# Kernel optimization log

Measured on AMD Instinct MI355X. Metric: run time of the kernel, lower is better.

## Reference

```python
import jax, jax.numpy as jnp
import numpy as np

VOCAB = 32000
D_MODEL = 1024


def setup_inputs() -> dict:
    key = jax.random.key(0)
    k = jax.random.split(key, 8)
    B, H, T, S = 8, 16, 128, 512
    src = jax.random.randint(k[0], (B, S), 0, VOCAB)
    decode_output = jax.random.normal(k[1], (B, T, D_MODEL), dtype=jnp.float32)
    decode_attn = jax.random.uniform(k[2], (B, H, T, S), dtype=jnp.float32)
    memory = jax.random.normal(k[3], (B, S, D_MODEL), dtype=jnp.float32)
    W_gen = jax.random.normal(k[4], (VOCAB, D_MODEL), dtype=jnp.float32) * (1.0 / np.sqrt(D_MODEL))
    b_gen = jnp.zeros((VOCAB,), dtype=jnp.float32)
    W_prob = jax.random.normal(k[5], (1, 2 * D_MODEL), dtype=jnp.float32) * (1.0 / np.sqrt(2 * D_MODEL))
    b_prob = jnp.zeros((1,), dtype=jnp.float32)
    return {"src": src, "decode_output": decode_output, "decode_attn": decode_attn,
            "memory": memory, "W_gen": W_gen, "b_gen": b_gen,
            "W_prob": W_prob, "b_prob": b_prob}


def reference(src, decode_output, decode_attn, memory, W_gen, b_gen, W_prob, b_prob):
    # mean over heads: [B, T, S]
    attn = jnp.mean(decode_attn, axis=1)
    B, T, S = attn.shape
    V = W_gen.shape[0]

    # generation logits: [B, T, V]
    gen_logits = jnp.einsum('btd,vd->btv', decode_output, W_gen) + b_gen

    # context vector: [B, T, D]
    context = jnp.einsum('bts,bsd->btd', attn, memory)

    # scatter-add copy distribution over vocab: [B, T, V]
    src_exp = jnp.broadcast_to(src[:, None, :], (B, T, S))  # token ids per step
    b_idx = jnp.arange(B)[:, None, None]
    t_idx = jnp.arange(T)[None, :, None]
    copy_logits = jnp.zeros((B, T, V), dtype=attn.dtype).at[b_idx, t_idx, src_exp].add(attn)

    # copy gate: sigmoid(Linear([context; decode_output])) -> [B, T, 1]
    cat = jnp.concatenate([context, decode_output], axis=-1)
    prob = jax.nn.sigmoid(jnp.einsum('btd,od->bto', cat, W_prob) + b_prob)

    gen_p = prob * jax.nn.softmax(gen_logits, axis=-1)
    copy_p = (1.0 - prob) * jax.nn.softmax(copy_logits, axis=-1)
    final = gen_p + copy_p
    return jnp.log(final).reshape(-1, V)
```

## Files before the change

kernel.cpp:

```cpp
#include <hip/hip_runtime.h>
#include <hip/hip_bf16.h>
#include <cstddef>
#include <cstdint>

#define BB 8
#define HH 16
#define TT 128
#define SS 512
#define DD 1024
#define VV 32000
#define MM (BB * TT)

typedef float f32x4 __attribute__((ext_vector_type(4)));
typedef short short8v __attribute__((ext_vector_type(8)));
typedef unsigned short ushort8v __attribute__((ext_vector_type(8)));

__device__ __forceinline__ unsigned short f2bf(float x) {
    __hip_bfloat16 h = __float2bfloat16(x);
    return __builtin_bit_cast(unsigned short, h);
}
__device__ __forceinline__ float bf2f(unsigned short u) {
    unsigned int x = ((unsigned int)u) << 16;
    return __builtin_bit_cast(float, x);
}

__device__ __forceinline__ float wave_sum(float v) {
#pragma unroll
    for (int o = 1; o < 64; o <<= 1) v += __shfl_xor(v, o);
    return v;
}
__device__ __forceinline__ float wave_max(float v) {
#pragma unroll
    for (int o = 1; o < 64; o <<= 1) v = fmaxf(v, __shfl_xor(v, o));
    return v;
}
__device__ __forceinline__ float block_sum(float v, float* red, int tid) {
    v = wave_sum(v);
    __syncthreads();
    if ((tid & 63) == 0) red[tid >> 6] = v;
    __syncthreads();
    return red[0] + red[1] + red[2] + red[3];
}
__device__ __forceinline__ float block_max(float v, float* red, int tid) {
    v = wave_max(v);
    __syncthreads();
    if ((tid & 63) == 0) red[tid >> 6] = v;
    __syncthreads();
    return fmaxf(fmaxf(red[0], red[1]), fmaxf(red[2], red[3]));
}

__global__ __launch_bounds__(512) void k_setup(const int* __restrict__ src,
                                               int* __restrict__ pos_map,
                                               const float* __restrict__ memory,
                                               const float* __restrict__ dec,
                                               const float* __restrict__ wprob,
                                               float* __restrict__ mw,
                                               float* __restrict__ dw,
                                               const float* __restrict__ wgen,
                                               unsigned short* __restrict__ Wbf,
                                               unsigned short* __restrict__ Abf) {
    int blk = blockIdx.x, tid = threadIdx.x;
    if (blk < 8) {
        int tok = src[blk * SS + tid];
        atomicMin(&pos_map[blk * VV + tok], tid);
    } else if (blk < 648) {
        int row = (blk - 8) * 8 + (tid >> 6);
        int lane = tid & 63;
        const float4* srcv;
        const float4* wv;
        if (row < BB * SS) {
            srcv = reinterpret_cast<const float4*>(memory + (size_t)row * DD);
            wv = reinterpret_cast<const float4*>(wprob);
        } else {
            srcv = reinterpret_cast<const float4*>(dec + (size_t)(row - BB * SS) * DD);
            wv = reinterpret_cast<const float4*>(wprob + DD);
        }
        float sum = 0.f;
#pragma unroll
        for (int k = 0; k < 4; ++k) {
            int idx = lane + 64 * k;
            float4 a = srcv[idx];
            float4 w = wv[idx];
            sum += a.x * w.x + a.y * w.y + a.z * w.z + a.w * w.w;
        }
        sum = wave_sum(sum);
        if (lane == 0) {
            if (row < BB * SS) mw[row] = sum;
            else dw[row - BB * SS] = sum;
        }
    } else if (blk < 1672) {
        if (Wbf == nullptr) return;
        const int n8 = VV * DD / 8;
        for (int i = (blk - 648) * 512 + tid; i < n8; i += 1024 * 512) {
            const float4* p = reinterpret_cast<const float4*>(wgen + (size_t)i * 8);
            float4 a = p[0], b = p[1];
            ushort8v u;
            u[0] = f2bf(a.x); u[1] = f2bf(a.y); u[2] = f2bf(a.z); u[3] = f2bf(a.w);
            u[4] = f2bf(b.x); u[5] = f2bf(b.y); u[6] = f2bf(b.z); u[7] = f2bf(b.w);
            *reinterpret_cast<ushort8v*>(Wbf + (size_t)i * 8) = u;
        }
    } else {
        if (Abf == nullptr) return;
        const int n8 = MM * DD / 8;
        for (int i = (blk - 1672) * 512 + tid; i < n8; i += 32 * 512) {
            const float4* p = reinterpret_cast<const float4*>(dec + (size_t)i * 8);
            float4 a = p[0], b = p[1];
            ushort8v u;
            u[0] = f2bf(a.x); u[1] = f2bf(a.y); u[2] = f2bf(a.z); u[3] = f2bf(a.w);
            u[4] = f2bf(b.x); u[5] = f2bf(b.y); u[6] = f2bf(b.z); u[7] = f2bf(b.w);
            *reinterpret_cast<ushort8v*>(Abf + (size_t)i * 8) = u;
        }
    }
}

#define NKT 32
#define BUFE 12288

#define AS1 __attribute__((address_space(1)))
#define AS3 __attribute__((address_space(3)))

template <int EPI>
__global__ __launch_bounds__(512, 4) void k_gemm_bf(const unsigned short* __restrict__ Abf,
                                                    const unsigned short* __restrict__ Wbf,
                                                    const float* __restrict__ bgen,
                                                    float* __restrict__ out,
                                                    unsigned short* __restrict__ ebuf,
                                                    float* __restrict__ zg) {
    __shared__ unsigned short lds[3 * BUFE];

    int tid = threadIdx.x;
    int p = blockIdx.x;
    int wgid = (p & 7) * 125 + (p >> 3);
    int mt = wgid & 7, nt = wgid >> 3;
    int m0 = mt * 128, v0 = nt * 256;

    int lane = tid & 63, w = tid >> 6;
    int wm = w & 1, wn = w >> 1;

    int srow = tid >> 2;
    int schunk = (tid & 3) ^ ((tid >> 3) & 3);
    const unsigned short* gA = Abf + (size_t)(m0 + srow) * DD + schunk * 8;
    const unsigned short* gB = Wbf + (size_t)(v0 + srow) * DD + schunk * 8;

#define STAGE(T, BI) do {                                                              \
    size_t ko_ = (size_t)(T) * 32;                                                     \
    __builtin_amdgcn_global_load_lds(                                                  \
        (const AS1 void*)(gA + ko_),                                                   \
        (AS3 void*)(lds + (BI) * BUFE + tid * 8), 16, 0, 0);                           \
    __builtin_amdgcn_global_load_lds(                                                  \
        (const AS1 void*)(gB + ko_),                                                   \
        (AS3 void*)(lds + (BI) * BUFE + 4096 + tid * 8), 16, 0, 0);                    \
    __builtin_amdgcn_global_load_lds(                                                  \
        (const AS1 void*)(gB + (size_t)128 * DD + ko_),                                \
        (AS3 void*)(lds + (BI) * BUFE + 8192 + tid * 8), 16, 0, 0);                    \
} while (0)

    int lr = lane & 15, kg = lane >> 4;
    int xr = (lr >> 1) & 3;
    const unsigned short* arow = lds + (wm * 64 + lr) * 32 + ((kg ^ xr) << 3);
    const unsigned short* brow = lds + 4096 + (wn * 64 + lr) * 32 + ((kg ^ xr) << 3);

    f32x4 acc[4][4] = {};

#define ITER(T, BI, DO_STAGE, VM)  do {                                                \
    __builtin_amdgcn_s_barrier();                                                      \
    short8v af[4], bfr[4];                                                             \
    _Pragma("unroll")                                                                  \
    for (int i = 0; i < 4; ++i) {                                                      \
        af[i] = *reinterpret_cast<const short8v*>(arow + (BI) * BUFE + i * 512);       \
        bfr[i] = *reinterpret_cast<const short8v*>(brow + (BI) * BUFE + i * 512);      \
    }                                                                                  \
    if (DO_STAGE) STAGE((T) + 2, ((BI) + 2) % 3);                                      \
    __builtin_amdgcn_s_setprio(1);                                                     \
    _Pragma("unroll")                                                                  \
    for (int i = 0; i < 4; ++i)                                                        \
        _Pragma("unroll")                                                              \
        for (int j = 0; j < 4; ++j)                                                    \
            acc[i][j] = __builtin_amdgcn_mfma_f32_16x16x32_bf16(af[i], bfr[j], acc[i][j], 0, 0, 0); \
    __builtin_amdgcn_s_setprio(0);                                                     \
    if ((VM) == 3) asm volatile("s_waitcnt vmcnt(3)" ::: "memory");                    \
    else if ((VM) == 0) asm volatile("s_waitcnt vmcnt(0)" ::: "memory");               \
} while (0)

    STAGE(0, 0);
    STAGE(1, 1);
    asm volatile("s_waitcnt vmcnt(3)" ::: "memory");

    for (int t = 0; t < NKT - 2; t += 3) {
        ITER(t + 0, 0, true, 3);
        ITER(t + 1, 1, true, 3);
        ITER(t + 2, 2, true, 3);
    }
    ITER(30, 0, false, 0);
    ITER(31, 1, false, -1);
#undef ITER
#undef STAGE

    int colb = lane & 15, rgrp = lane >> 4;
#pragma unroll
    for (int i = 0; i < 4; ++i) {
        float es0 = 0.f, es1 = 0.f, es2 = 0.f, es3 = 0.f;
        int gmb = m0 + wm * 64 + i * 16 + rgrp * 4;
#pragma unroll
        for (int j = 0; j < 4; ++j) {
            int gv = v0 + wn * 64 + j * 16 + colb;
            float bgj = bgen[gv];
            float v0f = acc[i][j][0] + bgj;
            float v1f = acc[i][j][1] + bgj;
            float v2f = acc[i][j][2] + bgj;
            float v3f = acc[i][j][3] + bgj;
            float e0 = __expf(v0f), e1 = __expf(v1f), e2 = __expf(v2f), e3 = __expf(v3f);
            if constexpr (EPI == 1) {
                ebuf[(size_t)(gmb + 0) * VV + gv] = f2bf(e0);
                ebuf[(size_t)(gmb + 1) * VV + gv] = f2bf(e1);
                ebuf[(size_t)(gmb + 2) * VV + gv] = f2bf(e2);
                ebuf[(size_t)(gmb + 3) * VV + gv] = f2bf(e3);
            } else {
                out[(size_t)(gmb + 0) * VV + gv] = v0f;
                out[(size_t)(gmb + 1) * VV + gv] = v1f;
                out[(size_t)(gmb + 2) * VV + gv] = v2f;
                out[(size_t)(gmb + 3) * VV + gv] = v3f;
            }
            es0 += e0; es1 += e1; es2 += e2; es3 += e3;
        }
        float es[4] = {es0, es1, es2, es3};
#pragma unroll
        for (int rr = 0; rr < 4; ++rr) {
            float e = es[rr];
            e += __shfl_xor(e, 1); e += __shfl_xor(e, 2);
            e += __shfl_xor(e, 4); e += __shfl_xor(e, 8);
            if (colb == 0) atomicAdd(&zg[gmb + rr], e);
        }
    }
}

#define FBb 128
#define FLDK 40

__global__ __launch_bounds__(256) void k_gemm_f32(const float* __restrict__ A,
                                                  const float* __restrict__ Wg,
                                                  const float* __restrict__ bgen,
                                                  float* __restrict__ out,
                                                  float* __restrict__ zg) {
    __shared__ unsigned short As[FBb * FLDK];
    __shared__ unsigned short Bs[FBb * FLDK];
    int tid = threadIdx.x;
    int bid = blockIdx.x;
    int mt = bid & 7;
    int nt = bid >> 3;
    int m0 = mt * FBb, v0 = nt * FBb;
    int lane = tid & 63, wid = tid >> 6;
    int wr = (wid >> 1) * 64, wc = (wid & 1) * 64;
    int lr = lane & 15, lk = (lane >> 4) << 3;
    int r = tid >> 1, c0 = (tid & 1) << 4;

    f32x4 acc[4][4] = {};

    for (int k0 = 0; k0 < DD; k0 += 32) {
        {
            const float4* pa = reinterpret_cast<const float4*>(A + (size_t)(m0 + r) * DD + k0 + c0);
            float4 x0 = pa[0], x1 = pa[1], x2 = pa[2], x3 = pa[3];
            ushort8v u0, u1;
            u0[0] = f2bf(x0.x); u0[1] = f2bf(x0.y); u0[2] = f2bf(x0.z); u0[3] = f2bf(x0.w);
            u0[4] = f2bf(x1.x); u0[5] = f2bf(x1.y); u0[6] = f2bf(x1.z); u0[7] = f2bf(x1.w);
            u1[0] = f2bf(x2.x); u1[1] = f2bf(x2.y); u1[2] = f2bf(x2.z); u1[3] = f2bf(x2.w);
            u1[4] = f2bf(x3.x); u1[5] = f2bf(x3.y); u1[6] = f2bf(x3.z); u1[7] = f2bf(x3.w);
            *reinterpret_cast<ushort8v*>(&As[r * FLDK + c0]) = u0;
            *reinterpret_cast<ushort8v*>(&As[r * FLDK + c0 + 8]) = u1;

            const float4* pb = reinterpret_cast<const float4*>(Wg + (size_t)(v0 + r) * DD + k0 + c0);
            float4 y0 = pb[0], y1 = pb[1], y2 = pb[2], y3 = pb[3];
            ushort8v w0, w1;
            w0[0] = f2bf(y0.x); w0[1] = f2bf(y0.y); w0[2] = f2bf(y0.z); w0[3] = f2bf(y0.w);
            w0[4] = f2bf(y1.x); w0[5] = f2bf(y1.y); w0[6] = f2bf(y1.z); w0[7] = f2bf(y1.w);
            w1[0] = f2bf(y2.x); w1[1] = f2bf(y2.y); w1[2] = f2bf(y2.z); w1[3] = f2bf(y2.w);
            w1[4] = f2bf(y3.x); w1[5] = f2bf(y3.y); w1[6] = f2bf(y3.z); w1[7] = f2bf(y3.w);
            *reinterpret_cast<ushort8v*>(&Bs[r * FLDK + c0]) = w0;
            *reinterpret_cast<ushort8v*>(&Bs[r * FLDK + c0 + 8]) = w1;
        }
        __syncthreads();

        short8v af[4], bfr[4];
#pragma unroll
        for (int i = 0; i < 4; ++i)
            af[i] = *reinterpret_cast<const short8v*>(&As[(wr + i * 16 + lr) * FLDK + lk]);
#pragma unroll
        for (int j = 0; j < 4; ++j)
            bfr[j] = *reinterpret_cast<const short8v*>(&Bs[(wc + j * 16 + lr) * FLDK + lk]);
#pragma unroll
        for (int i = 0; i < 4; ++i)
#pragma unroll
            for (int j = 0; j < 4; ++j)
                acc[i][j] = __builtin_amdgcn_mfma_f32_16x16x32_bf16(af[i], bfr[j], acc[i][j], 0, 0, 0);
        __syncthreads();
    }

    int colb = lane & 15;
    int rgrp = lane >> 4;
#pragma unroll
    for (int i = 0; i < 4; ++i) {
        float es0 = 0.f, es1 = 0.f, es2 = 0.f, es3 = 0.f;
        int gmb = m0 + wr + i * 16 + rgrp * 4;
#pragma unroll
        for (int j = 0; j < 4; ++j) {
            int gv = v0 + wc + j * 16 + colb;
            float bgj = bgen[gv];
            float v0f = acc[i][j][0] + bgj;
            float v1f = acc[i][j][1] + bgj;
            float v2f = acc[i][j][2] + bgj;
            float v3f = acc[i][j][3] + bgj;
            out[(size_t)(gmb + 0) * VV + gv] = v0f;
            out[(size_t)(gmb + 1) * VV + gv] = v1f;
            out[(size_t)(gmb + 2) * VV + gv] = v2f;
            out[(size_t)(gmb + 3) * VV + gv] = v3f;
            es0 += __expf(v0f); es1 += __expf(v1f);
            es2 += __expf(v2f); es3 += __expf(v3f);
        }
        float es[4] = {es0, es1, es2, es3};
#pragma unroll
        for (int rr = 0; rr < 4; ++rr) {
            float e = es[rr];
            e += __shfl_xor(e, 1); e += __shfl_xor(e, 2);
            e += __shfl_xor(e, 4); e += __shfl_xor(e, 8);
            if (colb == 0) atomicAdd(&zg[gmb + rr], e);
        }
    }
}

template <int RD16>
__global__ __launch_bounds__(256) void k_final(float* __restrict__ gen,
                                               const unsigned short* __restrict__ ebuf,
                                               const float* __restrict__ dattn,
                                               const int* __restrict__ src,
                                               const int* __restrict__ pos_map,
                                               const float* __restrict__ mw,
                                               const float* __restrict__ dw,
                                               const float* __restrict__ bprob,
                                               const float* __restrict__ zg) {
    int m = blockIdx.x;
    int b = m >> 7;
    int t = m & 127;
    int tid = threadIdx.x;
    __shared__ float a_row[SS];
    __shared__ float vals[SS];
    __shared__ int reps[SS];
    __shared__ float evs[SS];
    __shared__ float red[4];
    __shared__ float sA1, sA2, scc;

    {
        const float2* base = reinterpret_cast<const float2*>(
            dattn + ((size_t)b * HH * TT + t) * SS) + tid;
        float sx = 0.f, sy = 0.f;
#pragma unroll
        for (int h = 0; h < HH; ++h) {
            float2 v = base[(size_t)h * (TT * SS / 2)];
            sx += v.x; sy += v.y;
        }
        a_row[2 * tid] = sx * 0.0625f;
        a_row[2 * tid + 1] = sy * 0.0625f;
        vals[2 * tid] = 0.f;
        vals[2 * tid + 1] = 0.f;
    }
    {
        int s0 = 2 * tid, s1 = 2 * tid + 1;
        reps[s0] = pos_map[b * VV + src[b * SS + s0]];
        reps[s1] = pos_map[b * VV + src[b * SS + s1]];
    }
    __syncthreads();
    for (int s = tid; s < SS; s += 256) {
        atomicAdd(&vals[reps[s]], a_row[s]);
    }
    __syncthreads();
    float psum = 0.f;
    for (int s = tid; s < SS; s += 256) psum += a_row[s] * mw[b * SS + s];
    psum = block_sum(psum, red, tid);
    float z = psum + dw[m] + bprob[0];
    float p = 1.0f / (1.0f + __expf(-z));
    float mxv = -3.4e38f;
    for (int s = tid; s < SS; s += 256) {
        if (reps[s] == s) mxv = fmaxf(mxv, vals[s]);
    }
    mxv = block_max(mxv, red, tid);
    float m_c = fmaxf(0.0f, mxv);
    float sexp = 0.f, cnt = 0.f;
    for (int s = tid; s < SS; s += 256) {
        float e = 0.0f;
        if (reps[s] == s) {
            e = __expf(vals[s] - m_c);
            sexp += e;
            cnt += 1.0f;
        }
        evs[s] = e;
    }
    sexp = block_sum(sexp, red, tid);
    cnt = block_sum(cnt, red, tid);
    if (tid == 0) {
        float cc = __expf(-m_c);
        float zcv = ((float)VV - cnt) * cc + sexp;
        sA1 = p / zg[m];
        sA2 = (1.0f - p) / zcv;
        scc = cc;
    }
    __syncthreads();

    float A1 = sA1, A2 = sA2, cc = scc;
    float4* row = reinterpret_cast<float4*>(gen + (size_t)m * VV);
    const int4* pm = reinterpret_cast<const int4*>(pos_map + b * VV);
    if constexpr (RD16 == 1) {
        const ushort8v* erow = reinterpret_cast<const ushort8v*>(ebuf + (size_t)m * VV);
        for (int i = tid; i < VV / 8; i += 256) {
            ushort8v ee = erow[i];
            int4 rp0 = pm[2 * i], rp1 = pm[2 * i + 1];
            float4 o0, o1;
            o0.x = __logf(A1 * bf2f(ee[0]) + A2 * ((rp0.x < SS) ? evs[rp0.x] : cc));
            o0.y = __logf(A1 * bf2f(ee[1]) + A2 * ((rp0.y < SS) ? evs[rp0.y] : cc));
            o0.z = __logf(A1 * bf2f(ee[2]) + A2 * ((rp0.z < SS) ? evs[rp0.z] : cc));
            o0.w = __logf(A1 * bf2f(ee[3]) + A2 * ((rp0.w < SS) ? evs[rp0.w] : cc));
            o1.x = __logf(A1 * bf2f(ee[4]) + A2 * ((rp1.x < SS) ? evs[rp1.x] : cc));
            o1.y = __logf(A1 * bf2f(ee[5]) + A2 * ((rp1.y < SS) ? evs[rp1.y] : cc));
            o1.z = __logf(A1 * bf2f(ee[6]) + A2 * ((rp1.z < SS) ? evs[rp1.z] : cc));
            o1.w = __logf(A1 * bf2f(ee[7]) + A2 * ((rp1.w < SS) ? evs[rp1.w] : cc));
            row[2 * i] = o0;
            row[2 * i + 1] = o1;
        }
    } else {
        for (int i = tid; i < VV / 4; i += 256) {
            float4 g = row[i];
            int4 rp = pm[i];
            float4 o;
            o.x = __logf(A1 * __expf(g.x) + A2 * ((rp.x < SS) ? evs[rp.x] : cc));
            o.y = __logf(A1 * __expf(g.y) + A2 * ((rp.y < SS) ? evs[rp.y] : cc));
            o.z = __logf(A1 * __expf(g.z) + A2 * ((rp.z < SS) ? evs[rp.z] : cc));
            o.w = __logf(A1 * __expf(g.w) + A2 * ((rp.w < SS) ? evs[rp.w] : cc));
            row[i] = o;
        }
    }
}

extern "C" void kernel_launch(void* const* d_in, const int* in_sizes, int n_in,
                              void* d_out, int out_size, void* d_ws, size_t ws_size,
                              hipStream_t stream) {
    const int* src = (const int*)d_in[0];
    const float* dec = (const float*)d_in[1];
    const float* dattn = (const float*)d_in[2];
    const float* mem = (const float*)d_in[3];
    const float* wgen = (const float*)d_in[4];
    const float* bgen = (const float*)d_in[5];
    const float* wprob = (const float*)d_in[6];
    const float* bprob = (const float*)d_in[7];
    float* out = (float*)d_out;
    char* ws = (char*)d_ws;

    int* pos_map = (int*)(ws + 0);
    float* mw   = (float*)(ws + 1048576);
    float* dw   = (float*)(ws + 1048576 + 16384);
    float* zg   = (float*)(ws + 1048576 + 24576);
    unsigned short* Wbf = (unsigned short*)(ws + 1114112);
    unsigned short* Abf = (unsigned short*)(ws + 1114112 + 65536000);
    unsigned short* Ebf = (unsigned short*)(ws + 1114112 + 65536000 + 2097152);
    const size_t NEEDED  = 1114112ull + 65536000ull + 2097152ull;
    const size_t NEEDED2 = NEEDED + 65536000ull;

    bool do_cast = ws_size >= NEEDED;

    hipMemsetAsync(pos_map, 0x7F, (size_t)BB * VV * sizeof(int), stream);
    hipMemsetAsync(zg, 0, (size_t)MM * sizeof(float), stream);

    k_setup<<<do_cast ? 1704 : 648, 512, 0, stream>>>(
        src, pos_map, mem, dec, wprob, mw, dw, wgen,
        do_cast ? Wbf : nullptr, do_cast ? Abf : nullptr);

    if (do_cast) {
        if (ws_size >= NEEDED2) {
            k_gemm_bf<1><<<(MM / 128) * (VV / 256), 512, 0, stream>>>(Abf, Wbf, bgen, out, Ebf, zg);
            k_final<1><<<MM, 256, 0, stream>>>(out, Ebf, dattn, src, pos_map, mw, dw, bprob, zg);
        } else {
            k_gemm_bf<0><<<(MM / 128) * (VV / 256), 512, 0, stream>>>(Abf, Wbf, bgen, out, Ebf, zg);
            k_final<0><<<MM, 256, 0, stream>>>(out, Ebf, dattn, src, pos_map, mw, dw, bprob, zg);
        }
    } else {
        k_gemm_f32<<<(MM / FBb) * (VV / FBb), 256, 0, stream>>>(dec, wgen, bgen, out, zg);
        k_final<0><<<MM, 256, 0, stream>>>(out, Ebf, dattn, src, pos_map, mw, dw, bprob, zg);
    }
}
```

Measured before the change: 209.6 us.

## Shrink GEMM tile to 128x128 with 256 threads; widen final kernel to 512 threads

The bf16 GEMM moves from 512-thread blocks with 128x256 tiles to 256-thread blocks with 128x128 tiles. The LDS stage buffer shrinks accordingly, the A tile now takes two load instructions, and the vmcnt waits are adjusted. This doubles the grid and raises occupancy per CU, but each tile gets less reuse of the A operand. The final epilogue kernel switches to 512 threads, so each thread handles one source position, removing the strided loops and using 8-wave reductions.

```diff
diff --git a/kernel.cpp b/kernel.cpp
--- a/kernel.cpp
+++ b/kernel.cpp
@@ -34,19 +34,21 @@
     for (int o = 1; o < 64; o <<= 1) v = fmaxf(v, __shfl_xor(v, o));
     return v;
 }
-__device__ __forceinline__ float block_sum(float v, float* red, int tid) {
+__device__ __forceinline__ float block_sum8(float v, float* red, int tid) {
     v = wave_sum(v);
     __syncthreads();
     if ((tid & 63) == 0) red[tid >> 6] = v;
     __syncthreads();
-    return red[0] + red[1] + red[2] + red[3];
-}
-__device__ __forceinline__ float block_max(float v, float* red, int tid) {
+    return red[0] + red[1] + red[2] + red[3] + red[4] + red[5] + red[6] + red[7];
+}
+__device__ __forceinline__ float block_max8(float v, float* red, int tid) {
     v = wave_max(v);
     __syncthreads();
     if ((tid & 63) == 0) red[tid >> 6] = v;
     __syncthreads();
-    return fmaxf(fmaxf(red[0], red[1]), fmaxf(red[2], red[3]));
+    float a = fmaxf(fmaxf(red[0], red[1]), fmaxf(red[2], red[3]));
+    float b = fmaxf(fmaxf(red[4], red[5]), fmaxf(red[6], red[7]));
+    return fmaxf(a, b);
 }
 
 __global__ __launch_bounds__(512) void k_setup(const int* __restrict__ src,
@@ -114,13 +116,13 @@
 }
 
 #define NKT 32
-#define BUFE 12288
+#define BUFE 8192
 
 #define AS1 __attribute__((address_space(1)))
 #define AS3 __attribute__((address_space(3)))
 
 template <int EPI>
-__global__ __launch_bounds__(512, 4) void k_gemm_bf(const unsigned short* __restrict__ Abf,
+__global__ __launch_bounds__(256, 4) void k_gemm_bf(const unsigned short* __restrict__ Abf,
                                                     const unsigned short* __restrict__ Wbf,
                                                     const float* __restrict__ bgen,
                                                     float* __restrict__ out,
@@ -130,9 +132,9 @@
 
     int tid = threadIdx.x;
     int p = blockIdx.x;
-    int wgid = (p & 7) * 125 + (p >> 3);
+    int wgid = (p & 7) * 250 + (p >> 3);
     int mt = wgid & 7, nt = wgid >> 3;
-    int m0 = mt * 128, v0 = nt * 256;
+    int m0 = mt * 128, v0 = nt * 128;
 
     int lane = tid & 63, w = tid >> 6;
     int wm = w & 1, wn = w >> 1;
@@ -148,11 +150,14 @@
         (const AS1 void*)(gA + ko_),                                                   \
         (AS3 void*)(lds + (BI) * BUFE + tid * 8), 16, 0, 0);                           \
     __builtin_amdgcn_global_load_lds(                                                  \
+        (const AS1 void*)(gA + (size_t)64 * DD + ko_),                                 \
+        (AS3 void*)(lds + (BI) * BUFE + 2048 + tid * 8), 16, 0, 0);                    \
+    __builtin_amdgcn_global_load_lds(                                                  \
         (const AS1 void*)(gB + ko_),                                                   \
         (AS3 void*)(lds + (BI) * BUFE + 4096 + tid * 8), 16, 0, 0);                    \
     __builtin_amdgcn_global_load_lds(                                                  \
-        (const AS1 void*)(gB + (size_t)128 * DD + ko_),                                \
-        (AS3 void*)(lds + (BI) * BUFE + 8192 + tid * 8), 16, 0, 0);                    \
+        (const AS1 void*)(gB + (size_t)64 * DD + ko_),                                 \
+        (AS3 void*)(lds + (BI) * BUFE + 6144 + tid * 8), 16, 0, 0);                    \
 } while (0)
 
     int lr = lane & 15, kg = lane >> 4;
@@ -178,18 +183,18 @@
         for (int j = 0; j < 4; ++j)                                                    \
             acc[i][j] = __builtin_amdgcn_mfma_f32_16x16x32_bf16(af[i], bfr[j], acc[i][j], 0, 0, 0); \
     __builtin_amdgcn_s_setprio(0);                                                     \
-    if ((VM) == 3) asm volatile("s_waitcnt vmcnt(3)" ::: "memory");                    \
+    if ((VM) == 4) asm volatile("s_waitcnt vmcnt(4)" ::: "memory");                    \
     else if ((VM) == 0) asm volatile("s_waitcnt vmcnt(0)" ::: "memory");               \
 } while (0)
 
     STAGE(0, 0);
     STAGE(1, 1);
-    asm volatile("s_waitcnt vmcnt(3)" ::: "memory");
+    asm volatile("s_waitcnt vmcnt(4)" ::: "memory");
 
     for (int t = 0; t < NKT - 2; t += 3) {
-        ITER(t + 0, 0, true, 3);
-        ITER(t + 1, 1, true, 3);
-        ITER(t + 2, 2, true, 3);
+        ITER(t + 0, 0, true, 4);
+        ITER(t + 1, 1, true, 4);
+        ITER(t + 2, 2, true, 4);
     }
     ITER(30, 0, false, 0);
     ITER(31, 1, false, -1);
@@ -328,7 +333,7 @@
 }
 
 template <int RD16>
-__global__ __launch_bounds__(256) void k_final(float* __restrict__ gen,
+__global__ __launch_bounds__(512) void k_final(float* __restrict__ gen,
                                                const unsigned short* __restrict__ ebuf,
                                                const float* __restrict__ dattn,
                                                const int* __restrict__ src,
@@ -345,56 +350,40 @@
     __shared__ float vals[SS];
     __shared__ int reps[SS];
     __shared__ float evs[SS];
-    __shared__ float red[4];
+    __shared__ float red[8];
     __shared__ float sA1, sA2, scc;
 
     {
-        const float2* base = reinterpret_cast<const float2*>(
-            dattn + ((size_t)b * HH * TT + t) * SS) + tid;
-        float sx = 0.f, sy = 0.f;
-#pragma unroll
-        for (int h = 0; h < HH; ++h) {
-            float2 v = base[(size_t)h * (TT * SS / 2)];
-            sx += v.x; sy += v.y;
-        }
-        a_row[2 * tid] = sx * 0.0625f;
-        a_row[2 * tid + 1] = sy * 0.0625f;
-        vals[2 * tid] = 0.f;
-        vals[2 * tid + 1] = 0.f;
-    }
-    {
-        int s0 = 2 * tid, s1 = 2 * tid + 1;
-        reps[s0] = pos_map[b * VV + src[b * SS + s0]];
-        reps[s1] = pos_map[b * VV + src[b * SS + s1]];
-    }
-    __syncthreads();
-    for (int s = tid; s < SS; s += 256) {
-        atomicAdd(&vals[reps[s]], a_row[s]);
-    }
-    __syncthreads();
-    float psum = 0.f;
-    for (int s = tid; s < SS; s += 256) psum += a_row[s] * mw[b * SS + s];
-    psum = block_sum(psum, red, tid);
+        const float* base = dattn + ((size_t)b * HH * TT + t) * SS + tid;
+        float sx = 0.f;
+#pragma unroll
+        for (int h = 0; h < HH; ++h) sx += base[(size_t)h * (TT * SS)];
+        a_row[tid] = sx * 0.0625f;
+        vals[tid] = 0.f;
+        reps[tid] = pos_map[b * VV + src[b * SS + tid]];
+    }
+    __syncthreads();
+    atomicAdd(&vals[reps[tid]], a_row[tid]);
+    __syncthreads();
+    float psum = a_row[tid] * mw[b * SS + tid];
+    psum = block_sum8(psum, red, tid);
     float z = psum + dw[m] + bprob[0];
     float p = 1.0f / (1.0f + __expf(-z));
-    float mxv = -3.4e38f;
-    for (int s = tid; s < SS; s += 256) {
-        if (reps[s] == s) mxv = fmaxf(mxv, vals[s]);
-    }
-    mxv = block_max(mxv, red, tid);
+    float mxv = (reps[tid] == tid) ? vals[tid] : -3.4e38f;
+    mxv = block_max8(mxv, red, tid);
     float m_c = fmaxf(0.0f, mxv);
     float sexp = 0.f, cnt = 0.f;
-    for (int s = tid; s < SS; s += 256) {
+    {
         float e = 0.0f;
-        if (reps[s] == s) {
-            e = __expf(vals[s] - m_c);
-            sexp += e;
-            cnt += 1.0f;
-        }
-        evs[s] = e;
-    }
-    sexp = block_sum(sexp, red, tid);
-    cnt = block_sum(cnt, red, tid);
+        if (reps[tid] == tid) {
+            e = __expf(vals[tid] - m_c);
+            sexp = e;
+            cnt = 1.0f;
+        }
+        evs[tid] = e;
+    }
+    sexp = block_sum8(sexp, red, tid);
+    cnt = block_sum8(cnt, red, tid);
     if (tid == 0) {
         float cc = __expf(-m_c);
         float zcv = ((float)VV - cnt) * cc + sexp;
@@ -409,7 +398,7 @@
     const int4* pm = reinterpret_cast<const int4*>(pos_map + b * VV);
     if constexpr (RD16 == 1) {
         const ushort8v* erow = reinterpret_cast<const ushort8v*>(ebuf + (size_t)m * VV);
-        for (int i = tid; i < VV / 8; i += 256) {
+        for (int i = tid; i < VV / 8; i += 512) {
             ushort8v ee = erow[i];
             int4 rp0 = pm[2 * i], rp1 = pm[2 * i + 1];
             float4 o0, o1;
@@ -425,7 +414,7 @@
             row[2 * i + 1] = o1;
         }
     } else {
-        for (int i = tid; i < VV / 4; i += 256) {
+        for (int i = tid; i < VV / 4; i += 512) {
             float4 g = row[i];
             int4 rp = pm[i];
             float4 o;
@@ -473,14 +462,14 @@
 
     if (do_cast) {
         if (ws_size >= NEEDED2) {
-            k_gemm_bf<1><<<(MM / 128) * (VV / 256), 512, 0, stream>>>(Abf, Wbf, bgen, out, Ebf, zg);
-            k_final<1><<<MM, 256, 0, stream>>>(out, Ebf, dattn, src, pos_map, mw, dw, bprob, zg);
+            k_gemm_bf<1><<<(MM / 128) * (VV / 128), 256, 0, stream>>>(Abf, Wbf, bgen, out, Ebf, zg);
+            k_final<1><<<MM, 512, 0, stream>>>(out, Ebf, dattn, src, pos_map, mw, dw, bprob, zg);
         } else {
-            k_gemm_bf<0><<<(MM / 128) * (VV / 256), 512, 0, stream>>>(Abf, Wbf, bgen, out, Ebf, zg);
-            k_final<0><<<MM, 256, 0, stream>>>(out, Ebf, dattn, src, pos_map, mw, dw, bprob, zg);
+            k_gemm_bf<0><<<(MM / 128) * (VV / 128), 256, 0, stream>>>(Abf, Wbf, bgen, out, Ebf, zg);
+            k_final<0><<<MM, 512, 0, stream>>>(out, Ebf, dattn, src, pos_map, mw, dw, bprob, zg);
         }
     } else {
         k_gemm_f32<<<(MM / FBb) * (VV / FBb), 256, 0, stream>>>(dec, wgen, bgen, out, zg);
-        k_final<0><<<MM, 256, 0, stream>>>(out, Ebf, dattn, src, pos_map, mw, dw, bprob, zg);
-    }
-}
+        k_final<0><<<MM, 512, 0, stream>>>(out, Ebf, dattn, src, pos_map, mw, dw, bprob, zg);
+    }
+}
```

Measured after the change: 208.5 us. About the same (-0.5%).
